# Kernel tuning notes

Hardware: AMD Instinct MI355X
Metric: run time of the kernel (lower is better)

Reference implementation:

```python
import jax, jax.numpy as jnp
import numpy as np

ENCODER_DIM, DECODER_DIM, ATTN_DIM = 2048, 512, 512
B, P = 128, 196  # batch, num_pixels (14x14)


def setup_inputs() -> dict:
    key = jax.random.key(0)
    ks = jax.random.split(key, 8)
    s_e = 1.0 / np.sqrt(ENCODER_DIM)
    s_d = 1.0 / np.sqrt(DECODER_DIM)
    s_a = 1.0 / np.sqrt(ATTN_DIM)
    return {
        "encoder_out": jax.random.normal(ks[0], (B, P, ENCODER_DIM), jnp.float32),
        "decoder_hidden": jax.random.normal(ks[1], (B, DECODER_DIM), jnp.float32),
        "W_enc": jax.random.uniform(ks[2], (ENCODER_DIM, ATTN_DIM), jnp.float32, -s_e, s_e),
        "b_enc": jax.random.uniform(ks[3], (ATTN_DIM,), jnp.float32, -s_e, s_e),
        "W_dec": jax.random.uniform(ks[4], (DECODER_DIM, ATTN_DIM), jnp.float32, -s_d, s_d),
        "b_dec": jax.random.uniform(ks[5], (ATTN_DIM,), jnp.float32, -s_d, s_d),
        "W_full": jax.random.uniform(ks[6], (ATTN_DIM,), jnp.float32, -s_a, s_a),
        "b_full": jax.random.uniform(ks[7], (), jnp.float32, -s_a, s_a),
    }


def reference(encoder_out, decoder_hidden, W_enc, b_enc, W_dec, b_dec, W_full, b_full):
    # att1: [B, P, A]; att2: [B, A]
    att1 = jnp.einsum("bpe,ea->bpa", encoder_out, W_enc) + b_enc
    att2 = decoder_hidden @ W_dec + b_dec
    # broadcast add + relu + score projection -> [B, P]
    att = jax.nn.relu(att1 + att2[:, None, :]) @ W_full + b_full
    alpha = jax.nn.softmax(att, axis=1)  # over pixels
    # weighted sum over pixels -> [B, E]
    attention_weighted_encoding = jnp.einsum("bpe,bp->be", encoder_out, alpha)
    return (attention_weighted_encoding, alpha)
```

## Files before the change

kernel.cpp:

```cpp
#include <hip/hip_runtime.h>
#include <hip/hip_bf16.h>

#define ENC_DIM 2048
#define DEC_DIM 512
#define ATT_DIM 512
#define BATCH   128
#define NPIX    196
#define NROWS   (BATCH * NPIX)

typedef short bf16x8 __attribute__((ext_vector_type(8)));
typedef float f32x4  __attribute__((ext_vector_type(4)));
typedef unsigned short u16x8 __attribute__((ext_vector_type(8)));

__device__ __forceinline__ unsigned short f2bf(float f) {
    union { float f; unsigned u; } v; v.f = f;
    unsigned r = v.u + 0x7fffu + ((v.u >> 16) & 1u);
    return (unsigned short)(r >> 16);
}

__device__ __forceinline__ short bfc(float f) {
    union { __hip_bfloat16 h; short s; } v;
    v.h = __float2bfloat16(f);
    return v.s;
}

__device__ __forceinline__ void gload16(const void* g, void* l) {
    __builtin_amdgcn_global_load_lds(
        (const __attribute__((address_space(1))) unsigned int*)g,
        (__attribute__((address_space(3))) unsigned int*)l, 16, 0, 0);
}

__global__ void k0_transpose(const float* __restrict__ W_enc,
                             unsigned short* __restrict__ Wt) {
    __shared__ float ts[64][65];
    const int a0 = blockIdx.x * 64;
    const int e0 = blockIdx.y * 64;
    const int tx = threadIdx.x & 15;
    const int ty = threadIdx.x >> 4;
    #pragma unroll
    for (int p = 0; p < 4; ++p) {
        const int e = ty + p * 16;
        const float4 v = *(const float4*)&W_enc[(size_t)(e0 + e) * ATT_DIM + a0 + tx * 4];
        ts[e][tx * 4 + 0] = v.x; ts[e][tx * 4 + 1] = v.y;
        ts[e][tx * 4 + 2] = v.z; ts[e][tx * 4 + 3] = v.w;
    }
    __syncthreads();
    #pragma unroll
    for (int p = 0; p < 4; ++p) {
        const int a = ty + p * 16;
        ushort4 u;
        u.x = f2bf(ts[tx * 4 + 0][a]);
        u.y = f2bf(ts[tx * 4 + 1][a]);
        u.z = f2bf(ts[tx * 4 + 2][a]);
        u.w = f2bf(ts[tx * 4 + 3][a]);
        *(ushort4*)&Wt[(size_t)(a0 + a) * ENC_DIM + e0 + tx * 4] = u;
    }
}

__global__ void k1_att2(const float* __restrict__ dh, const float* __restrict__ W_dec,
                        const float* __restrict__ b_dec, const float* __restrict__ b_enc,
                        const float* __restrict__ b_full,
                        float* __restrict__ att2, float* __restrict__ score) {
    __shared__ float dhs[DEC_DIM];
    const int bid = blockIdx.x, t = threadIdx.x;
    const int b = bid >> 1;
    const int c = (bid & 1) * 256 + t;
    dhs[t]       = dh[b * DEC_DIM + t];
    dhs[t + 256] = dh[b * DEC_DIM + t + 256];
    __syncthreads();
    float acc0 = 0.f, acc1 = 0.f;
    #pragma unroll 8
    for (int d = 0; d < 256; ++d) {
        acc0 += dhs[d]       * W_dec[d * ATT_DIM + c];
        acc1 += dhs[d + 256] * W_dec[(d + 256) * ATT_DIM + c];
    }
    att2[b * ATT_DIM + c] = acc0 + acc1 + b_dec[c] + b_enc[c];
    const int gid = bid * 256 + t;
    if (gid < NROWS) score[gid] = b_full[0];
}

__launch_bounds__(256, 3)
__global__ void k2_gemm(const float* __restrict__ enc, const unsigned short* __restrict__ Wt,
                        const float* __restrict__ att2, const float* __restrict__ W_full,
                        float* __restrict__ score) {
    __shared__ __align__(16) float          Asf[128 * 64];
    __shared__ __align__(16) unsigned short Bs [128 * 64];
    __shared__ float att2s[2][128];
    __shared__ float wfs[128];

    const int t = threadIdx.x;
    const int tile = (blockIdx.x & 7) * 98 + (blockIdx.x >> 3);
    const int n0   = (tile & 3) * 128;
    const int row0 = (tile >> 2) * 128;
    const int b0   = row0 / NPIX;
    const int rows_left = (b0 + 1) * NPIX - row0;

    if (t < 128) {
        att2s[0][t] = att2[b0 * ATT_DIM + n0 + t];
        att2s[1][t] = (b0 + 1 < BATCH) ? att2[(b0 + 1) * ATT_DIM + n0 + t] : 0.f;
        wfs[t]      = W_full[n0 + t];
    }

    const int w    = t >> 6;
    const int lane = t & 63;
    const int q    = lane >> 4;
    const int cl   = lane & 15;
    const int wm   = (w >> 1) * 64;
    const int wn   = (w & 1) * 64;

    f32x4 acc[4][4] = {};

    const int r4 = lane >> 4;
    const int sl = lane & 15;
    const float* aS0 = enc + (size_t)(row0 + w * 32 + r4)     * ENC_DIM + ((sl ^ r4)       << 2);
    const float* aS1 = enc + (size_t)(row0 + w * 32 + 4 + r4) * ENC_DIM + ((sl ^ (4 + r4)) << 2);

    const int br = lane >> 3;
    const int bc = ((lane & 7) ^ br) * 8;
    const unsigned short* WtB = Wt + (size_t)(n0 + w * 32 + br) * ENC_DIM + bc;

    unsigned ab[4], ab2[4];
    #pragma unroll
    for (int mi = 0; mi < 4; ++mi) {
        unsigned base = ((unsigned)(wm + mi * 16 + cl) << 8) + ((unsigned)(cl & 7) << 4);
        base ^= (unsigned)(q << 5);
        ab[mi]  = base;
        ab2[mi] = base ^ 16u;
    }
    const char* Ab = (const char*)Asf;

    for (int kk = 0; kk < ENC_DIM; kk += 64) {
        __syncthreads();
        #pragma unroll
        for (int i = 0; i < 4; ++i)
            gload16(WtB + (size_t)i * 8 * ENC_DIM + kk, &Bs[(w * 32 + i * 8) * 64]);
        #pragma unroll
        for (int i = 0; i < 4; ++i) {
            gload16(aS0 + (size_t)i * 8 * ENC_DIM + kk, &Asf[(w * 32 + i * 8)     * 64]);
            gload16(aS1 + (size_t)i * 8 * ENC_DIM + kk, &Asf[(w * 32 + i * 8 + 4) * 64]);
        }
        __syncthreads();

        #pragma unroll
        for (int h = 0; h < 2; ++h) {
            bf16x8 af[4], bfr[4];
            #pragma unroll
            for (int mi = 0; mi < 4; ++mi) {
                const f32x4 fa = *(const f32x4*)(Ab + ab[mi]  + h * 128);
                const f32x4 fb = *(const f32x4*)(Ab + ab2[mi] + h * 128);
                bf16x8 u;
                u[0] = bfc(fa[0]); u[1] = bfc(fa[1]); u[2] = bfc(fa[2]); u[3] = bfc(fa[3]);
                u[4] = bfc(fb[0]); u[5] = bfc(fb[1]); u[6] = bfc(fb[2]); u[7] = bfc(fb[3]);
                af[mi] = u;
            }
            #pragma unroll
            for (int i = 0; i < 4; ++i)
                bfr[i] = *(const bf16x8*)&Bs[(wn + i * 16 + cl) * 64
                                             + (((h * 4 + q) ^ (cl & 7)) * 8)];
            #pragma unroll
            for (int mi = 0; mi < 4; ++mi)
                #pragma unroll
                for (int ni = 0; ni < 4; ++ni)
                    acc[mi][ni] = __builtin_amdgcn_mfma_f32_16x16x32_bf16(
                        af[mi], bfr[ni], acc[mi][ni], 0, 0, 0);
        }
    }

    #pragma unroll
    for (int mi = 0; mi < 4; ++mi) {
        float rs[4];
        #pragma unroll
        for (int i = 0; i < 4; ++i) {
            const int lr  = wm + mi * 16 + q * 4 + i;
            const int sel = (lr >= rows_left) ? 1 : 0;
            float sum = 0.f;
            #pragma unroll
            for (int ni = 0; ni < 4; ++ni) {
                const int j = wn + ni * 16 + cl;
                float v = acc[mi][ni][i] + att2s[sel][j];
                v = fmaxf(v, 0.f);
                sum += v * wfs[j];
            }
            rs[i] = sum;
        }
        #pragma unroll
        for (int o = 1; o < 16; o <<= 1) {
            #pragma unroll
            for (int i = 0; i < 4; ++i) rs[i] += __shfl_xor(rs[i], o);
        }
        if (cl == 0) {
            #pragma unroll
            for (int i = 0; i < 4; ++i) {
                const int r = row0 + wm + mi * 16 + q * 4 + i;
                atomicAdd(&score[r], rs[i]);
            }
        }
    }
}

__global__ void k4_awe(const float* __restrict__ enc, const float* __restrict__ score,
                       float* __restrict__ alpha, float* __restrict__ awe) {
    __shared__ float as[NPIX];
    __shared__ float red[4];
    __shared__ f32x4 redv[4][64];
    const int b  = blockIdx.y;
    const int t  = threadIdx.x;
    const int wv = t >> 6, lane = t & 63;
    const float x = (t < NPIX) ? score[b * NPIX + t] : -INFINITY;
    float m = x;
    #pragma unroll
    for (int o = 32; o >= 1; o >>= 1) m = fmaxf(m, __shfl_xor(m, o));
    if (lane == 0) red[wv] = m;
    __syncthreads();
    m = fmaxf(fmaxf(red[0], red[1]), fmaxf(red[2], red[3]));
    const float e = (t < NPIX) ? __expf(x - m) : 0.f;
    float s = e;
    #pragma unroll
    for (int o = 32; o >= 1; o >>= 1) s += __shfl_xor(s, o);
    __syncthreads();
    if (lane == 0) red[wv] = s;
    __syncthreads();
    s = red[0] + red[1] + red[2] + red[3];
    const float a = e / s;
    if (t < NPIX) {
        as[t] = a;
        if (blockIdx.x == 0) alpha[b * NPIX + t] = a;
    }
    __syncthreads();
    const int e0 = blockIdx.x * 256 + lane * 4;
    const float* base = enc + (size_t)b * NPIX * ENC_DIM + e0;
    f32x4 a0 = {}, a1 = {}, a2 = {}, a3 = {};
    int p = wv;
    #pragma unroll 4
    for (int it = 0; it < 12; ++it, p += 16) {
        a0 += as[p]      * *(const f32x4*)(base + (size_t)(p)      * ENC_DIM);
        a1 += as[p + 4]  * *(const f32x4*)(base + (size_t)(p + 4)  * ENC_DIM);
        a2 += as[p + 8]  * *(const f32x4*)(base + (size_t)(p + 8)  * ENC_DIM);
        a3 += as[p + 12] * *(const f32x4*)(base + (size_t)(p + 12) * ENC_DIM);
    }
    a0 += as[p] * *(const f32x4*)(base + (size_t)p * ENC_DIM);
    redv[wv][lane] = (a0 + a1) + (a2 + a3);
    __syncthreads();
    if (wv == 0) {
        const f32x4 r = (redv[0][lane] + redv[1][lane]) + (redv[2][lane] + redv[3][lane]);
        *(f32x4*)&awe[(size_t)b * ENC_DIM + e0] = r;
    }
}

extern "C" void kernel_launch(void* const* d_in, const int* in_sizes, int n_in,
                              void* d_out, int out_size, void* d_ws, size_t ws_size,
                              hipStream_t stream) {
    const float* enc    = (const float*)d_in[0];
    const float* dh     = (const float*)d_in[1];
    const float* W_enc  = (const float*)d_in[2];
    const float* b_enc  = (const float*)d_in[3];
    const float* W_dec  = (const float*)d_in[4];
    const float* b_dec  = (const float*)d_in[5];
    const float* W_full = (const float*)d_in[6];
    const float* b_full = (const float*)d_in[7];

    float* awe   = (float*)d_out;
    float* alpha = awe + BATCH * ENC_DIM;

    unsigned short* Wt    = (unsigned short*)d_ws;
    float*          att2  = (float*)((char*)d_ws + (size_t)ATT_DIM * ENC_DIM * 2);
    float*          score = att2 + (size_t)BATCH * ATT_DIM;

    k0_transpose<<<dim3(8, 32),  256, 0, stream>>>(W_enc, Wt);
    k1_att2     <<<256,          256, 0, stream>>>(dh, W_dec, b_dec, b_enc, b_full, att2, score);
    k2_gemm     <<<784,          256, 0, stream>>>(enc, Wt, att2, W_full, score);
    k4_awe      <<<dim3(8, 128), 256, 0, stream>>>(enc, score, alpha, awe);
}
```

Before: 396.1 us.

## Double-buffer GEMM tiles with register prefetch and bf16 A staging in LDS

The GEMM main loop now prefetches the next K-slice of the encoder activations into registers and of the transposed weights via async LDS loads, while the current slice is being computed. Activations are converted to bf16 once when written to a padded LDS tile, instead of being stored as fp32 and converted by every wave. This is meant to overlap global memory latency with MFMA work and halve LDS traffic for the A operand. In exchange it double-buffers LDS, holds more prefetch registers, and drops occupancy from 3 to 2 blocks per CU.

Measured after the change: 447.6 us. +13.0%, slower.

```diff
diff --git a/kernel.cpp b/kernel.cpp
--- a/kernel.cpp
+++ b/kernel.cpp
@@ -18,10 +18,10 @@
     return (unsigned short)(r >> 16);
 }
 
-__device__ __forceinline__ short bfc(float f) {
-    union { __hip_bfloat16 h; short s; } v;
+__device__ __forceinline__ unsigned short bfc(float f) {
+    union { __hip_bfloat16 h; unsigned short u; } v;
     v.h = __float2bfloat16(f);
-    return v.s;
+    return v.u;
 }
 
 __device__ __forceinline__ void gload16(const void* g, void* l) {
@@ -79,12 +79,12 @@
     if (gid < NROWS) score[gid] = b_full[0];
 }
 
-__launch_bounds__(256, 3)
+__launch_bounds__(256, 2)
 __global__ void k2_gemm(const float* __restrict__ enc, const unsigned short* __restrict__ Wt,
                         const float* __restrict__ att2, const float* __restrict__ W_full,
                         float* __restrict__ score) {
-    __shared__ __align__(16) float          Asf[128 * 64];
-    __shared__ __align__(16) unsigned short Bs [128 * 64];
+    __shared__ __align__(16) unsigned short As[2][128 * 72];
+    __shared__ __align__(16) unsigned short Bs[2][128 * 64];
     __shared__ float att2s[2][128];
     __shared__ float wfs[128];
 
@@ -110,60 +110,81 @@
 
     f32x4 acc[4][4] = {};
 
-    const int r4 = lane >> 4;
-    const int sl = lane & 15;
-    const float* aS0 = enc + (size_t)(row0 + w * 32 + r4)     * ENC_DIM + ((sl ^ r4)       << 2);
-    const float* aS1 = enc + (size_t)(row0 + w * 32 + 4 + r4) * ENC_DIM + ((sl ^ (4 + r4)) << 2);
+    const int ar = t >> 3;
+    const int ak = (t & 7) * 8;
+    const float* encA = enc + (size_t)(row0 + ar) * ENC_DIM + ak;
 
     const int br = lane >> 3;
     const int bc = ((lane & 7) ^ br) * 8;
     const unsigned short* WtB = Wt + (size_t)(n0 + w * 32 + br) * ENC_DIM + bc;
 
-    unsigned ab[4], ab2[4];
-    #pragma unroll
-    for (int mi = 0; mi < 4; ++mi) {
-        unsigned base = ((unsigned)(wm + mi * 16 + cl) << 8) + ((unsigned)(cl & 7) << 4);
-        base ^= (unsigned)(q << 5);
-        ab[mi]  = base;
-        ab2[mi] = base ^ 16u;
-    }
-    const char* Ab = (const char*)Asf;
-
-    for (int kk = 0; kk < ENC_DIM; kk += 64) {
-        __syncthreads();
+    {
         #pragma unroll
         for (int i = 0; i < 4; ++i)
-            gload16(WtB + (size_t)i * 8 * ENC_DIM + kk, &Bs[(w * 32 + i * 8) * 64]);
-        #pragma unroll
-        for (int i = 0; i < 4; ++i) {
-            gload16(aS0 + (size_t)i * 8 * ENC_DIM + kk, &Asf[(w * 32 + i * 8)     * 64]);
-            gload16(aS1 + (size_t)i * 8 * ENC_DIM + kk, &Asf[(w * 32 + i * 8 + 4) * 64]);
-        }
-        __syncthreads();
+            gload16(WtB + (size_t)i * 8 * ENC_DIM, &Bs[0][(w * 32 + i * 8) * 64]);
+        #pragma unroll
+        for (int p = 0; p < 4; ++p) {
+            const float4 v0 = *(const float4*)(encA + (size_t)p * 32 * ENC_DIM);
+            const float4 v1 = *(const float4*)(encA + (size_t)p * 32 * ENC_DIM + 4);
+            u16x8 u;
+            u[0] = bfc(v0.x); u[1] = bfc(v0.y); u[2] = bfc(v0.z); u[3] = bfc(v0.w);
+            u[4] = bfc(v1.x); u[5] = bfc(v1.y); u[6] = bfc(v1.z); u[7] = bfc(v1.w);
+            *(u16x8*)&As[0][(ar + p * 32) * 72 + ak] = u;
+        }
+    }
+    __syncthreads();
+
+    int cur = 0;
+    for (int kk = 0; kk < ENC_DIM; kk += 64, cur ^= 1) {
+        const int  nxt = cur ^ 1;
+        const bool pf  = (kk + 64 < ENC_DIM);
+        float4 aL[8];
+
+        if (pf) {
+            #pragma unroll
+            for (int p = 0; p < 4; ++p) {
+                aL[2 * p]     = *(const float4*)(encA + (size_t)p * 32 * ENC_DIM + kk + 64);
+                aL[2 * p + 1] = *(const float4*)(encA + (size_t)p * 32 * ENC_DIM + kk + 68);
+            }
+            #pragma unroll
+            for (int i = 0; i < 4; ++i)
+                gload16(WtB + (size_t)i * 8 * ENC_DIM + kk + 64,
+                        &Bs[nxt][(w * 32 + i * 8) * 64]);
+        }
 
         #pragma unroll
         for (int h = 0; h < 2; ++h) {
             bf16x8 af[4], bfr[4];
             #pragma unroll
-            for (int mi = 0; mi < 4; ++mi) {
-                const f32x4 fa = *(const f32x4*)(Ab + ab[mi]  + h * 128);
-                const f32x4 fb = *(const f32x4*)(Ab + ab2[mi] + h * 128);
-                bf16x8 u;
-                u[0] = bfc(fa[0]); u[1] = bfc(fa[1]); u[2] = bfc(fa[2]); u[3] = bfc(fa[3]);
-                u[4] = bfc(fb[0]); u[5] = bfc(fb[1]); u[6] = bfc(fb[2]); u[7] = bfc(fb[3]);
-                af[mi] = u;
-            }
-            #pragma unroll
             for (int i = 0; i < 4; ++i)
-                bfr[i] = *(const bf16x8*)&Bs[(wn + i * 16 + cl) * 64
-                                             + (((h * 4 + q) ^ (cl & 7)) * 8)];
-            #pragma unroll
-            for (int mi = 0; mi < 4; ++mi)
+                af[i]  = *(const bf16x8*)&As[cur][(wm + i * 16 + cl) * 72 + h * 32 + q * 8];
+            #pragma unroll
+            for (int i = 0; i < 4; ++i)
+                bfr[i] = *(const bf16x8*)&Bs[cur][(wn + i * 16 + cl) * 64
+                                                  + (((h * 4 + q) ^ (cl & 7)) * 8)];
+            #pragma unroll
+            for (int mi = 0; mi < 2; ++mi)
                 #pragma unroll
-                for (int ni = 0; ni < 4; ++ni)
-                    acc[mi][ni] = __builtin_amdgcn_mfma_f32_16x16x32_bf16(
-                        af[mi], bfr[ni], acc[mi][ni], 0, 0, 0);
-        }
+                for (int ni = 0; ni < 4; ++ni) {
+                    acc[mi][ni]     = __builtin_amdgcn_mfma_f32_16x16x32_bf16(
+                        af[mi],     bfr[ni], acc[mi][ni],     0, 0, 0);
+                    acc[mi + 2][ni] = __builtin_amdgcn_mfma_f32_16x16x32_bf16(
+                        af[mi + 2], bfr[ni], acc[mi + 2][ni], 0, 0, 0);
+                }
+        }
+
+        if (pf) {
+            #pragma unroll
+            for (int p = 0; p < 4; ++p) {
+                u16x8 u;
+                u[0] = bfc(aL[2*p].x);   u[1] = bfc(aL[2*p].y);
+                u[2] = bfc(aL[2*p].z);   u[3] = bfc(aL[2*p].w);
+                u[4] = bfc(aL[2*p+1].x); u[5] = bfc(aL[2*p+1].y);
+                u[6] = bfc(aL[2*p+1].z); u[7] = bfc(aL[2*p+1].w);
+                *(u16x8*)&As[nxt][(ar + p * 32) * 72 + ak] = u;
+            }
+        }
+        __syncthreads();
     }
 
     #pragma unroll
```

## Merge prep kernels and fuse softmax and weighted sum into GEMM tail

Applied to the files above, without the earlier changes.

Combines the W_enc transpose/bf16 conversion and the att2 projection into one prep kernel that also zeroes per-batch counters. The GEMM kernel now counts finished tiles per batch with atomics, and the last tile to finish a batch runs that batch's softmax and attention-weighted sum. This drops two launches and the standalone awe pass, and aims to reuse encoder data while it may still be in cache. The cost is that each batch's 196x2048 reduction is done by a single 256-thread block, which can leave a serial tail at the end of the grid.

Result: slower. 553.0 us (+39.6%).

```diff
diff --git a/kernel.cpp b/kernel.cpp
--- a/kernel.cpp
+++ b/kernel.cpp
@@ -30,63 +30,71 @@
         (__attribute__((address_space(3))) unsigned int*)l, 16, 0, 0);
 }
 
-__global__ void k0_transpose(const float* __restrict__ W_enc,
-                             unsigned short* __restrict__ Wt) {
+__global__ void prep(const float* __restrict__ W_enc, const float* __restrict__ dh,
+                     const float* __restrict__ W_dec, const float* __restrict__ b_dec,
+                     const float* __restrict__ b_enc, const float* __restrict__ b_full,
+                     unsigned short* __restrict__ Wt, float* __restrict__ att2,
+                     float* __restrict__ score, int* __restrict__ cnt) {
     __shared__ float ts[64][65];
-    const int a0 = blockIdx.x * 64;
-    const int e0 = blockIdx.y * 64;
-    const int tx = threadIdx.x & 15;
-    const int ty = threadIdx.x >> 4;
-    #pragma unroll
-    for (int p = 0; p < 4; ++p) {
-        const int e = ty + p * 16;
-        const float4 v = *(const float4*)&W_enc[(size_t)(e0 + e) * ATT_DIM + a0 + tx * 4];
-        ts[e][tx * 4 + 0] = v.x; ts[e][tx * 4 + 1] = v.y;
-        ts[e][tx * 4 + 2] = v.z; ts[e][tx * 4 + 3] = v.w;
-    }
-    __syncthreads();
-    #pragma unroll
-    for (int p = 0; p < 4; ++p) {
-        const int a = ty + p * 16;
-        ushort4 u;
-        u.x = f2bf(ts[tx * 4 + 0][a]);
-        u.y = f2bf(ts[tx * 4 + 1][a]);
-        u.z = f2bf(ts[tx * 4 + 2][a]);
-        u.w = f2bf(ts[tx * 4 + 3][a]);
-        *(ushort4*)&Wt[(size_t)(a0 + a) * ENC_DIM + e0 + tx * 4] = u;
-    }
-}
-
-__global__ void k1_att2(const float* __restrict__ dh, const float* __restrict__ W_dec,
-                        const float* __restrict__ b_dec, const float* __restrict__ b_enc,
-                        const float* __restrict__ b_full,
-                        float* __restrict__ att2, float* __restrict__ score) {
-    __shared__ float dhs[DEC_DIM];
     const int bid = blockIdx.x, t = threadIdx.x;
-    const int b = bid >> 1;
-    const int c = (bid & 1) * 256 + t;
-    dhs[t]       = dh[b * DEC_DIM + t];
-    dhs[t + 256] = dh[b * DEC_DIM + t + 256];
-    __syncthreads();
-    float acc0 = 0.f, acc1 = 0.f;
-    #pragma unroll 8
-    for (int d = 0; d < 256; ++d) {
-        acc0 += dhs[d]       * W_dec[d * ATT_DIM + c];
-        acc1 += dhs[d + 256] * W_dec[(d + 256) * ATT_DIM + c];
-    }
-    att2[b * ATT_DIM + c] = acc0 + acc1 + b_dec[c] + b_enc[c];
-    const int gid = bid * 256 + t;
-    if (gid < NROWS) score[gid] = b_full[0];
+
+    if (bid < 98) {
+        const int gid = bid * 256 + t;
+        score[gid] = b_full[0];
+    }
+    if (bid == 0 && t < BATCH) cnt[t] = 0;
+
+    if (bid < 256) {
+        const int a0 = (bid & 7) * 64;
+        const int e0 = (bid >> 3) * 64;
+        const int tx = t & 15;
+        const int ty = t >> 4;
+        #pragma unroll
+        for (int p = 0; p < 4; ++p) {
+            const int e = ty + p * 16;
+            const float4 v = *(const float4*)&W_enc[(size_t)(e0 + e) * ATT_DIM + a0 + tx * 4];
+            ts[e][tx * 4 + 0] = v.x; ts[e][tx * 4 + 1] = v.y;
+            ts[e][tx * 4 + 2] = v.z; ts[e][tx * 4 + 3] = v.w;
+        }
+        __syncthreads();
+        #pragma unroll
+        for (int p = 0; p < 4; ++p) {
+            const int a = ty + p * 16;
+            ushort4 u;
+            u.x = f2bf(ts[tx * 4 + 0][a]);
+            u.y = f2bf(ts[tx * 4 + 1][a]);
+            u.z = f2bf(ts[tx * 4 + 2][a]);
+            u.w = f2bf(ts[tx * 4 + 3][a]);
+            *(ushort4*)&Wt[(size_t)(a0 + a) * ENC_DIM + e0 + tx * 4] = u;
+        }
+    } else {
+        float* dhs = &ts[0][0];
+        const int kb = bid - 256;
+        const int b  = kb >> 1;
+        const int c  = (kb & 1) * 256 + t;
+        dhs[t]       = dh[b * DEC_DIM + t];
+        dhs[t + 256] = dh[b * DEC_DIM + t + 256];
+        __syncthreads();
+        float acc0 = 0.f, acc1 = 0.f;
+        #pragma unroll 8
+        for (int d = 0; d < 256; ++d) {
+            acc0 += dhs[d]       * W_dec[d * ATT_DIM + c];
+            acc1 += dhs[d + 256] * W_dec[(d + 256) * ATT_DIM + c];
+        }
+        att2[b * ATT_DIM + c] = acc0 + acc1 + b_dec[c] + b_enc[c];
+    }
 }
 
 __launch_bounds__(256, 3)
-__global__ void k2_gemm(const float* __restrict__ enc, const unsigned short* __restrict__ Wt,
-                        const float* __restrict__ att2, const float* __restrict__ W_full,
-                        float* __restrict__ score) {
+__global__ void k2g(const float* __restrict__ enc, const unsigned short* __restrict__ Wt,
+                    const float* __restrict__ att2, const float* __restrict__ W_full,
+                    float* __restrict__ score, int* __restrict__ cnt,
+                    float* __restrict__ alpha, float* __restrict__ awe) {
     __shared__ __align__(16) float          Asf[128 * 64];
     __shared__ __align__(16) unsigned short Bs [128 * 64];
     __shared__ float att2s[2][128];
     __shared__ float wfs[128];
+    __shared__ int   finb[2];
 
     const int t = threadIdx.x;
     const int tile = (blockIdx.x & 7) * 98 + (blockIdx.x >> 3);
@@ -196,54 +204,68 @@
             }
         }
     }
-}
-
-__global__ void k4_awe(const float* __restrict__ enc, const float* __restrict__ score,
-                       float* __restrict__ alpha, float* __restrict__ awe) {
-    __shared__ float as[NPIX];
-    __shared__ float red[4];
-    __shared__ f32x4 redv[4][64];
-    const int b  = blockIdx.y;
-    const int t  = threadIdx.x;
-    const int wv = t >> 6, lane = t & 63;
-    const float x = (t < NPIX) ? score[b * NPIX + t] : -INFINITY;
-    float m = x;
+
+    __threadfence();
+    __syncthreads();
+    if (t == 0) {
+        finb[0] = -1; finb[1] = -1;
+        {
+            const int first = (b0 * NPIX) >> 7, last = (b0 * NPIX + NPIX - 1) >> 7;
+            if (atomicAdd(&cnt[b0], 1) + 1 == 4 * (last - first + 1)) finb[0] = b0;
+        }
+        if (rows_left < 128) {
+            const int b1 = b0 + 1;
+            const int first = (b1 * NPIX) >> 7, last = (b1 * NPIX + NPIX - 1) >> 7;
+            if (atomicAdd(&cnt[b1], 1) + 1 == 4 * (last - first + 1)) finb[1] = b1;
+        }
+    }
+    __syncthreads();
+
     #pragma unroll
-    for (int o = 32; o >= 1; o >>= 1) m = fmaxf(m, __shfl_xor(m, o));
-    if (lane == 0) red[wv] = m;
-    __syncthreads();
-    m = fmaxf(fmaxf(red[0], red[1]), fmaxf(red[2], red[3]));
-    const float e = (t < NPIX) ? __expf(x - m) : 0.f;
-    float s = e;
-    #pragma unroll
-    for (int o = 32; o >= 1; o >>= 1) s += __shfl_xor(s, o);
-    __syncthreads();
-    if (lane == 0) red[wv] = s;
-    __syncthreads();
-    s = red[0] + red[1] + red[2] + red[3];
-    const float a = e / s;
-    if (t < NPIX) {
-        as[t] = a;
-        if (blockIdx.x == 0) alpha[b * NPIX + t] = a;
-    }
-    __syncthreads();
-    const int e0 = blockIdx.x * 256 + lane * 4;
-    const float* base = enc + (size_t)b * NPIX * ENC_DIM + e0;
-    f32x4 a0 = {}, a1 = {}, a2 = {}, a3 = {};
-    int p = wv;
-    #pragma unroll 4
-    for (int it = 0; it < 12; ++it, p += 16) {
-        a0 += as[p]      * *(const f32x4*)(base + (size_t)(p)      * ENC_DIM);
-        a1 += as[p + 4]  * *(const f32x4*)(base + (size_t)(p + 4)  * ENC_DIM);
-        a2 += as[p + 8]  * *(const f32x4*)(base + (size_t)(p + 8)  * ENC_DIM);
-        a3 += as[p + 12] * *(const f32x4*)(base + (size_t)(p + 12) * ENC_DIM);
-    }
-    a0 += as[p] * *(const f32x4*)(base + (size_t)p * ENC_DIM);
-    redv[wv][lane] = (a0 + a1) + (a2 + a3);
-    __syncthreads();
-    if (wv == 0) {
-        const f32x4 r = (redv[0][lane] + redv[1][lane]) + (redv[2][lane] + redv[3][lane]);
-        *(f32x4*)&awe[(size_t)b * ENC_DIM + e0] = r;
+    for (int j = 0; j < 2; ++j) {
+        const int fb = finb[j];
+        if (fb < 0) continue;
+        float* sA  = (float*)Bs;
+        float* red = &att2s[0][0];
+        const int wv = t >> 6;
+        const float x = (t < NPIX)
+            ? __hip_atomic_load(&score[fb * NPIX + t], __ATOMIC_RELAXED,
+                                __HIP_MEMORY_SCOPE_AGENT)
+            : -INFINITY;
+        float m = x;
+        #pragma unroll
+        for (int o = 32; o >= 1; o >>= 1) m = fmaxf(m, __shfl_xor(m, o));
+        if (lane == 0) red[wv] = m;
+        __syncthreads();
+        m = fmaxf(fmaxf(red[0], red[1]), fmaxf(red[2], red[3]));
+        const float e = (t < NPIX) ? __expf(x - m) : 0.f;
+        float s = e;
+        #pragma unroll
+        for (int o = 32; o >= 1; o >>= 1) s += __shfl_xor(s, o);
+        __syncthreads();
+        if (lane == 0) red[wv] = s;
+        __syncthreads();
+        s = red[0] + red[1] + red[2] + red[3];
+        const float a = e / s;
+        if (t < NPIX) {
+            sA[t] = a;
+            alpha[fb * NPIX + t] = a;
+        }
+        __syncthreads();
+        const int c0 = t * 8;
+        const float* base = enc + (size_t)fb * NPIX * ENC_DIM;
+        f32x4 s0a = {}, s0b = {}, s1a = {}, s1b = {};
+        #pragma unroll 4
+        for (int p = 0; p < NPIX; p += 2) {
+            const float w0 = sA[p], w1 = sA[p + 1];
+            s0a += w0 * *(const f32x4*)(base + (size_t)p       * ENC_DIM + c0);
+            s1a += w0 * *(const f32x4*)(base + (size_t)p       * ENC_DIM + c0 + 4);
+            s0b += w1 * *(const f32x4*)(base + (size_t)(p + 1) * ENC_DIM + c0);
+            s1b += w1 * *(const f32x4*)(base + (size_t)(p + 1) * ENC_DIM + c0 + 4);
+        }
+        *(f32x4*)&awe[(size_t)fb * ENC_DIM + c0]     = s0a + s0b;
+        *(f32x4*)&awe[(size_t)fb * ENC_DIM + c0 + 4] = s1a + s1b;
+        __syncthreads();
     }
 }
 
@@ -265,9 +287,9 @@
     unsigned short* Wt    = (unsigned short*)d_ws;
     float*          att2  = (float*)((char*)d_ws + (size_t)ATT_DIM * ENC_DIM * 2);
     float*          score = att2 + (size_t)BATCH * ATT_DIM;
-
-    k0_transpose<<<dim3(8, 32),  256, 0, stream>>>(W_enc, Wt);
-    k1_att2     <<<256,          256, 0, stream>>>(dh, W_dec, b_dec, b_enc, b_full, att2, score);
-    k2_gemm     <<<784,          256, 0, stream>>>(enc, Wt, att2, W_full, score);
-    k4_awe      <<<dim3(8, 128), 256, 0, stream>>>(enc, score, alpha, awe);
-}
+    int*            cnt   = (int*)(score + NROWS);
+
+    prep<<<512, 256, 0, stream>>>(W_enc, dh, W_dec, b_dec, b_enc, b_full,
+                                  Wt, att2, score, cnt);
+    k2g <<<784, 256, 0, stream>>>(enc, Wt, att2, W_full, score, cnt, alpha, awe);
+}
```
